# Kernel tuning notes

Hardware: AMD Instinct MI355X
Metric: run time of the kernel (lower is better)

Reference implementation:

```python
import jax, jax.numpy as jnp
import numpy as np

S = 3072      # total tokens across all images
DIM = 1280    # hidden_size
H = 16        # num_heads
HD = DIM // H # head_dim = 80
NSEG = 6      # number of images (cu_seqlens has NSEG+1 entries)


def _rotate_half(x):
    x1, x2 = jnp.split(x, 2, axis=-1)
    return jnp.concatenate([-x2, x1], axis=-1)


def setup_inputs() -> dict:
    key = jax.random.key(0)
    ks = jax.random.split(key, 12)
    hidden_states = jax.random.normal(ks[0], (S, DIM), jnp.float32)
    # realistic vision rotary embedding: half-dim inv_freq, repeated to head_dim
    inv_freq = 1.0 / (10000.0 ** (jnp.arange(0, HD // 2, dtype=jnp.float32) / (HD // 2)))
    freqs = jnp.arange(S, dtype=jnp.float32)[:, None] * inv_freq[None, :]  # [S, HD/2]
    emb = jnp.concatenate([freqs, freqs], axis=-1)  # [S, HD]
    cos = jnp.cos(emb)
    sin = jnp.sin(emb)
    sc = 0.02
    wq = jax.random.normal(ks[1], (DIM, DIM), jnp.float32) * sc
    bq = jax.random.normal(ks[2], (DIM,), jnp.float32) * sc
    wk = jax.random.normal(ks[3], (DIM, DIM), jnp.float32) * sc
    bk = jax.random.normal(ks[4], (DIM,), jnp.float32) * sc
    wv = jax.random.normal(ks[5], (DIM, DIM), jnp.float32) * sc
    bv = jax.random.normal(ks[6], (DIM,), jnp.float32) * sc
    wo = jax.random.normal(ks[7], (DIM, DIM), jnp.float32) * sc
    bo = jax.random.normal(ks[8], (DIM,), jnp.float32) * sc
    cu_seqlens = (jnp.arange(NSEG + 1, dtype=jnp.int32) * (S // NSEG))  # [0,512,...,3072]
    return dict(hidden_states=hidden_states, cos=cos, sin=sin,
                wq=wq, bq=bq, wk=wk, bk=bk, wv=wv, bv=bv, wo=wo, bo=bo,
                cu_seqlens=cu_seqlens)


def reference(hidden_states, cos, sin, wq, bq, wk, bk, wv, bv, wo, bo, cu_seqlens):
    seq_length = hidden_states.shape[0]
    scaling = HD ** (-0.5)
    # QKV projections (torch Linear: x @ W.T + b)
    q = (hidden_states @ wq.T + bq).reshape(seq_length, H, HD)
    k = (hidden_states @ wk.T + bk).reshape(seq_length, H, HD)
    v = (hidden_states @ wv.T + bv).reshape(seq_length, H, HD)
    # apply_rotary_pos_emb_vision: cos/sin [S, HD] broadcast over head axis
    c = cos[:, None, :]
    s = sin[:, None, :]
    q = q * c + _rotate_half(q) * s
    k = k * c + _rotate_half(k) * s
    # block-diagonal (per-image) attention via segment mask
    seg = jnp.searchsorted(cu_seqlens[1:], jnp.arange(seq_length), side='right')
    mask = seg[:, None] == seg[None, :]  # [S, S] bool
    scores = jnp.einsum('shd,thd->hst', q, k) * scaling  # [H, S, S]
    scores = jnp.where(mask[None, :, :], scores, jnp.finfo(scores.dtype).min)
    attn = jax.nn.softmax(scores, axis=-1)
    out = jnp.einsum('hst,thd->shd', attn, v).reshape(seq_length, DIM)
    return out @ wo.T + bo
```

## Files before the change

kernel.cpp:

```cpp
#include <hip/hip_runtime.h>
#include <hip/hip_bf16.h>
#include <hip/hip_fp16.h>
#include <cstdint>
#include <cstddef>

typedef _Float16 f16;
typedef f16 f16x2 __attribute__((ext_vector_type(2)));
typedef f16 f16x4 __attribute__((ext_vector_type(4)));
typedef f16 f16x8 __attribute__((ext_vector_type(8)));
typedef float f32x4 __attribute__((ext_vector_type(4)));

#define S_LEN 3072
#define DIM 1280
#define NH 16
#define HD 80
#define SEG 512

#define MFMA16F(a, b, c) __builtin_amdgcn_mfma_f32_16x16x32_f16((a), (b), (c), 0, 0, 0)

__device__ __forceinline__ void gl2lds16(const void* g, void* l) {
    __builtin_amdgcn_global_load_lds(
        (const __attribute__((address_space(1))) unsigned int*)g,
        (__attribute__((address_space(3))) unsigned int*)l, 16, 0, 0);
}

__device__ __forceinline__ unsigned int pack2(float a, float b) {
    f16x2 t = {(f16)a, (f16)b};
    union { f16x2 v; unsigned int u; } c;
    c.v = t;
    return c.u;
}

__global__ __launch_bounds__(256) void cvt_kernel(
    const float* __restrict__ hs,
    const float* __restrict__ wq, const float* __restrict__ wk,
    const float* __restrict__ wv, const float* __restrict__ wo,
    f16* __restrict__ hs16,
    f16* __restrict__ wq16, f16* __restrict__ wk16,
    f16* __restrict__ wv16, f16* __restrict__ wo16)
{
    const int m = blockIdx.y;
    const float* src; f16* dst; int n4;
    if (m == 0)      { src = hs; dst = hs16; n4 = S_LEN * DIM / 4; }
    else if (m == 1) { src = wq; dst = wq16; n4 = DIM * DIM / 4; }
    else if (m == 2) { src = wk; dst = wk16; n4 = DIM * DIM / 4; }
    else if (m == 3) { src = wv; dst = wv16; n4 = DIM * DIM / 4; }
    else             { src = wo; dst = wo16; n4 = DIM * DIM / 4; }
    int idx = blockIdx.x * 256 + threadIdx.x;
    if (idx >= n4) return;
    f32x4 v = *(const f32x4*)(src + (size_t)idx * 4);
    f16x4 o;
#pragma unroll
    for (int e = 0; e < 4; ++e) o[e] = (f16)v[e];
    *(f16x4*)(dst + (size_t)idx * 4) = o;
}

__global__ __launch_bounds__(512, 2) void gemm_qkv192(
    const f16* __restrict__ A, const f16* __restrict__ Wb,
    const float* __restrict__ bq, const float* __restrict__ bk,
    const float* __restrict__ bv,
    f16* __restrict__ q16, f16* __restrict__ k16, f16* __restrict__ vT)
{
    const int bid = blockIdx.x;
    const int xcd = bid & 7;
    const int idx = bid >> 3;
    const int mt = xcd * 2 + idx / 15;
    const int nt = idx % 15;
    const int m0 = mt * 192;
    const int n0 = nt * 256;

    __shared__ __align__(16) f16 Abuf[2][192 * 64];
    __shared__ __align__(16) f16 Bbuf[2][256 * 64];

    const int tid = threadIdx.x;
    const int w = tid >> 6;
    const int lane = tid & 63;
    const int lane15 = lane & 15;
    const int quad = lane >> 4;
    const int wm = (w >> 2) * 96;
    const int wn = (w & 3) * 64;

    const int srow = lane >> 3;
    const int schk = (lane & 7) ^ srow;

    const int aRow = w * 24;
    const int bRow = (w & 3) * 64 + (w >> 2) * 16;

    const f16* gA = A + (size_t)(m0 + aRow + srow) * DIM + schk * 8;
    const f16* gB = Wb + (size_t)(n0 + bRow + srow) * DIM + schk * 8;

    const int x7 = lane15 & 7;
    const int cc0 = (quad ^ x7) * 8;
    const int cc1 = ((quad + 4) ^ x7) * 8;

    f32x4 acc[6][4];
#pragma unroll
    for (int i = 0; i < 6; ++i)
#pragma unroll
        for (int j = 0; j < 4; ++j)
            acc[i][j] = (f32x4){0.f, 0.f, 0.f, 0.f};

    {
        f16* lB = Bbuf[0] + bRow * 64;
        gl2lds16(gB, lB);
        gl2lds16(gB + 8 * DIM, lB + 512);
        gl2lds16(gB + 32 * DIM, lB + 2048);
        gl2lds16(gB + 40 * DIM, lB + 2560);
        f16* lA = Abuf[0] + aRow * 64;
        gl2lds16(gA, lA);
        gl2lds16(gA + 8 * DIM, lA + 512);
        gl2lds16(gA + 16 * DIM, lA + 1024);
        f16* lB1 = Bbuf[1] + bRow * 64;
        gl2lds16(gB + 64, lB1);
        gl2lds16(gB + 8 * DIM + 64, lB1 + 512);
        gl2lds16(gB + 32 * DIM + 64, lB1 + 2048);
        gl2lds16(gB + 40 * DIM + 64, lB1 + 2560);
        f16* lA1 = Abuf[1] + aRow * 64;
        gl2lds16(gA + 64, lA1);
        gl2lds16(gA + 8 * DIM + 64, lA1 + 512);
        gl2lds16(gA + 16 * DIM + 64, lA1 + 1024);
    }
    asm volatile("s_waitcnt vmcnt(7)" ::: "memory");
    __builtin_amdgcn_s_barrier();

    f16x8 a0[3][2], a1[3][2], b01[2][2], b23[2][2];
#pragma unroll
    for (int i = 0; i < 3; ++i) {
        const f16* rp = Abuf[0] + (wm + i * 16 + lane15) * 64;
        a0[i][0] = *(const f16x8*)(rp + cc0);
        a0[i][1] = *(const f16x8*)(rp + cc1);
    }
#pragma unroll
    for (int j = 0; j < 2; ++j) {
        const f16* rp = Bbuf[0] + (wn + j * 16 + lane15) * 64;
        b01[j][0] = *(const f16x8*)(rp + cc0);
        b01[j][1] = *(const f16x8*)(rp + cc1);
    }

    for (int kt = 0; kt < 20; ++kt) {
        const int s = kt & 1;
        const int sn = s ^ 1;
        const int k2 = (kt + 2 < 20) ? kt + 2 : 19;
        const f16* As = Abuf[s];
        const f16* Bsl = Bbuf[s];
        const f16* Asn = Abuf[sn];
        const f16* Bsn = Bbuf[sn];
        const f16* gA2 = gA + k2 * 64;
        const f16* gB2 = gB + k2 * 64;

        __builtin_amdgcn_s_barrier();
        asm volatile("s_waitcnt lgkmcnt(0)" ::: "memory");
        __builtin_amdgcn_sched_barrier(0);
        __builtin_amdgcn_s_setprio(1);
#pragma unroll
        for (int i = 0; i < 3; ++i)
#pragma unroll
            for (int j = 0; j < 2; ++j) {
                acc[i][j] = MFMA16F(a0[i][0], b01[j][0], acc[i][j]);
                acc[i][j] = MFMA16F(a0[i][1], b01[j][1], acc[i][j]);
            }
        __builtin_amdgcn_s_setprio(0);
        __builtin_amdgcn_sched_barrier(0);
#pragma unroll
        for (int j = 0; j < 2; ++j) {
            const f16* rp = Bsl + (wn + 32 + j * 16 + lane15) * 64;
            b23[j][0] = *(const f16x8*)(rp + cc0);
            b23[j][1] = *(const f16x8*)(rp + cc1);
        }

        __builtin_amdgcn_s_barrier();
        asm volatile("s_waitcnt lgkmcnt(0)" ::: "memory");
        __builtin_amdgcn_sched_barrier(0);
        __builtin_amdgcn_s_setprio(1);
#pragma unroll
        for (int i = 0; i < 3; ++i)
#pragma unroll
            for (int j = 0; j < 2; ++j) {
                acc[i][j + 2] = MFMA16F(a0[i][0], b23[j][0], acc[i][j + 2]);
                acc[i][j + 2] = MFMA16F(a0[i][1], b23[j][1], acc[i][j + 2]);
            }
        __builtin_amdgcn_s_setprio(0);
        __builtin_amdgcn_sched_barrier(0);
#pragma unroll
        for (int i = 0; i < 3; ++i) {
            const f16* rp = As + (wm + 48 + i * 16 + lane15) * 64;
            a1[i][0] = *(const f16x8*)(rp + cc0);
            a1[i][1] = *(const f16x8*)(rp + cc1);
        }
        {
            f16* lB = Bbuf[s] + bRow * 64;
            gl2lds16(gB2, lB);
            gl2lds16(gB2 + 8 * DIM, lB + 512);
            gl2lds16(gB2 + 32 * DIM, lB + 2048);
            gl2lds16(gB2 + 40 * DIM, lB + 2560);
        }
        asm volatile("s_waitcnt vmcnt(4)" ::: "memory");

        __builtin_amdgcn_s_barrier();
        asm volatile("s_waitcnt lgkmcnt(0)" ::: "memory");
        __builtin_amdgcn_sched_barrier(0);
        __builtin_amdgcn_s_setprio(1);
#pragma unroll
        for (int i = 0; i < 3; ++i)
#pragma unroll
            for (int j = 0; j < 2; ++j) {
                acc[i + 3][j + 2] = MFMA16F(a1[i][0], b23[j][0], acc[i + 3][j + 2]);
                acc[i + 3][j + 2] = MFMA16F(a1[i][1], b23[j][1], acc[i + 3][j + 2]);
            }
        __builtin_amdgcn_s_setprio(0);
        __builtin_amdgcn_sched_barrier(0);
#pragma unroll
        for (int i = 0; i < 3; ++i) {
            const f16* rp = Asn + (wm + i * 16 + lane15) * 64;
            a0[i][0] = *(const f16x8*)(rp + cc0);
            a0[i][1] = *(const f16x8*)(rp + cc1);
        }
        {
            f16* lA = Abuf[s] + aRow * 64;
            gl2lds16(gA2, lA);
            gl2lds16(gA2 + 8 * DIM, lA + 512);
            gl2lds16(gA2 + 16 * DIM, lA + 1024);
        }

        __builtin_amdgcn_s_barrier();
        asm volatile("s_waitcnt lgkmcnt(0)" ::: "memory");
        __builtin_amdgcn_sched_barrier(0);
        __builtin_amdgcn_s_setprio(1);
#pragma unroll
        for (int i = 0; i < 3; ++i)
#pragma unroll
            for (int j = 0; j < 2; ++j) {
                acc[i + 3][j] = MFMA16F(a1[i][0], b01[j][0], acc[i + 3][j]);
                acc[i + 3][j] = MFMA16F(a1[i][1], b01[j][1], acc[i + 3][j]);
            }
        __builtin_amdgcn_s_setprio(0);
        __builtin_amdgcn_sched_barrier(0);
#pragma unroll
        for (int j = 0; j < 2; ++j) {
            const f16* rp = Bsn + (wn + j * 16 + lane15) * 64;
            b01[j][0] = *(const f16x8*)(rp + cc0);
            b01[j][1] = *(const f16x8*)(rp + cc1);
        }
    }
    asm volatile("s_waitcnt vmcnt(0) lgkmcnt(0)" ::: "memory");

    const int sel = nt / 5;
    const int nc0 = (nt % 5) * 256 + wn;
    const float* bias = (sel == 0) ? bq : (sel == 1) ? bk : bv;
    float bvv[4];
#pragma unroll
    for (int j = 0; j < 4; ++j) bvv[j] = bias[nc0 + j * 16 + lane15];

    if (sel < 2) {
        f16* O = sel ? k16 : q16;
#pragma unroll
        for (int i = 0; i < 6; ++i)
#pragma unroll
            for (int j = 0; j < 4; ++j)
#pragma unroll
                for (int r = 0; r < 4; ++r) {
                    int row = m0 + wm + i * 16 + quad * 4 + r;
                    O[(size_t)row * DIM + nc0 + j * 16 + lane15] =
                        (f16)(acc[i][j][r] + bvv[j]);
                }
    } else {
#pragma unroll
        for (int i = 0; i < 6; ++i)
#pragma unroll
            for (int j = 0; j < 4; ++j) {
                f16x4 ov;
#pragma unroll
                for (int r = 0; r < 4; ++r) ov[r] = (f16)(acc[i][j][r] + bvv[j]);
                int row = m0 + wm + i * 16 + quad * 4;
                int col = nc0 + j * 16 + lane15;
                *(f16x4*)(vT + (size_t)col * S_LEN + row) = ov;
            }
    }
}

__global__ __launch_bounds__(256, 2) void gemm_out_kernel(
    const f16* __restrict__ A, const f16* __restrict__ W,
    const float* __restrict__ bias, float* __restrict__ OF)
{
    const int bid = blockIdx.x;
    const int xcd = bid & 7;
    const int idx = bid >> 3;
    const int mt = xcd * 3 + idx / 10;
    const int nt = idx % 10;
    const int m0 = mt * 128;
    const int n0 = nt * 128;

    __shared__ __align__(16) f16 Abuf[2][128 * 64];
    __shared__ __align__(16) f16 Bbuf[2][128 * 64];

    const int tid = threadIdx.x;
    const int w = tid >> 6;
    const int lane = tid & 63;
    const int lane15 = lane & 15;
    const int quad = lane >> 4;
    const int wm = (w >> 1) * 64;
    const int wn = (w & 1) * 64;

    const int srow = lane >> 3;
    const int schk = (lane & 7) ^ srow;

    const int aRow = w * 32;
    const int bRow = w * 32;

    const f16* gA = A + (size_t)(m0 + aRow + srow) * DIM + schk * 8;
    const f16* gB = W + (size_t)(n0 + bRow + srow) * DIM + schk * 8;

    const int x7 = lane15 & 7;
    const int cc0 = (quad ^ x7) * 8;
    const int cc1 = ((quad + 4) ^ x7) * 8;

    f32x4 acc[4][4];
#pragma unroll
    for (int i = 0; i < 4; ++i)
#pragma unroll
        for (int j = 0; j < 4; ++j)
            acc[i][j] = (f32x4){0.f, 0.f, 0.f, 0.f};

    {
        f16* lB = Bbuf[0] + bRow * 64;
        gl2lds16(gB, lB);
        gl2lds16(gB + 8 * DIM, lB + 512);
        gl2lds16(gB + 16 * DIM, lB + 1024);
        gl2lds16(gB + 24 * DIM, lB + 1536);
        f16* lA = Abuf[0] + aRow * 64;
        gl2lds16(gA, lA);
        gl2lds16(gA + 8 * DIM, lA + 512);
        gl2lds16(gA + 16 * DIM, lA + 1024);
        gl2lds16(gA + 24 * DIM, lA + 1536);
        f16* lB1 = Bbuf[1] + bRow * 64;
        gl2lds16(gB + 64, lB1);
        gl2lds16(gB + 8 * DIM + 64, lB1 + 512);
        gl2lds16(gB + 16 * DIM + 64, lB1 + 1024);
        gl2lds16(gB + 24 * DIM + 64, lB1 + 1536);
        f16* lA1 = Abuf[1] + aRow * 64;
        gl2lds16(gA + 64, lA1);
        gl2lds16(gA + 8 * DIM + 64, lA1 + 512);
        gl2lds16(gA + 16 * DIM + 64, lA1 + 1024);
        gl2lds16(gA + 24 * DIM + 64, lA1 + 1536);
    }
    asm volatile("s_waitcnt vmcnt(8)" ::: "memory");
    __builtin_amdgcn_s_barrier();

    f16x8 a0[2][2], a1[2][2], b01[2][2], b23[2][2];
#pragma unroll
    for (int i = 0; i < 2; ++i) {
        const f16* rp = Abuf[0] + (wm + i * 16 + lane15) * 64;
        a0[i][0] = *(const f16x8*)(rp + cc0);
        a0[i][1] = *(const f16x8*)(rp + cc1);
    }
#pragma unroll
    for (int j = 0; j < 2; ++j) {
        const f16* rp = Bbuf[0] + (wn + j * 16 + lane15) * 64;
        b01[j][0] = *(const f16x8*)(rp + cc0);
        b01[j][1] = *(const f16x8*)(rp + cc1);
    }

    for (int kt = 0; kt < 20; ++kt) {
        const int s = kt & 1;
        const int sn = s ^ 1;
        const int k2 = (kt + 2 < 20) ? kt + 2 : 19;
        const f16* As = Abuf[s];
        const f16* Bsl = Bbuf[s];
        const f16* Asn = Abuf[sn];
        const f16* Bsn = Bbuf[sn];
        const f16* gA2 = gA + k2 * 64;
        const f16* gB2 = gB + k2 * 64;

        __builtin_amdgcn_s_barrier();
        asm volatile("s_waitcnt lgkmcnt(0)" ::: "memory");
        __builtin_amdgcn_sched_barrier(0);
        __builtin_amdgcn_s_setprio(1);
#pragma unroll
        for (int i = 0; i < 2; ++i)
#pragma unroll
            for (int j = 0; j < 2; ++j) {
                acc[i][j] = MFMA16F(a0[i][0], b01[j][0], acc[i][j]);
                acc[i][j] = MFMA16F(a0[i][1], b01[j][1], acc[i][j]);
            }
        __builtin_amdgcn_s_setprio(0);
        __builtin_amdgcn_sched_barrier(0);
#pragma unroll
        for (int j = 0; j < 2; ++j) {
            const f16* rp = Bsl + (wn + 32 + j * 16 + lane15) * 64;
            b23[j][0] = *(const f16x8*)(rp + cc0);
            b23[j][1] = *(const f16x8*)(rp + cc1);
        }

        __builtin_amdgcn_s_barrier();
        asm volatile("s_waitcnt lgkmcnt(0)" ::: "memory");
        __builtin_amdgcn_sched_barrier(0);
        __builtin_amdgcn_s_setprio(1);
#pragma unroll
        for (int i = 0; i < 2; ++i)
#pragma unroll
            for (int j = 0; j < 2; ++j) {
                acc[i][j + 2] = MFMA16F(a0[i][0], b23[j][0], acc[i][j + 2]);
                acc[i][j + 2] = MFMA16F(a0[i][1], b23[j][1], acc[i][j + 2]);
            }
        __builtin_amdgcn_s_setprio(0);
        __builtin_amdgcn_sched_barrier(0);
#pragma unroll
        for (int i = 0; i < 2; ++i) {
            const f16* rp = As + (wm + 32 + i * 16 + lane15) * 64;
            a1[i][0] = *(const f16x8*)(rp + cc0);
            a1[i][1] = *(const f16x8*)(rp + cc1);
        }
        {
            f16* lB = Bbuf[s] + bRow * 64;
            gl2lds16(gB2, lB);
            gl2lds16(gB2 + 8 * DIM, lB + 512);
            gl2lds16(gB2 + 16 * DIM, lB + 1024);
            gl2lds16(gB2 + 24 * DIM, lB + 1536);
        }
        asm volatile("s_waitcnt vmcnt(4)" ::: "memory");

        __builtin_amdgcn_s_barrier();
        asm volatile("s_waitcnt lgkmcnt(0)" ::: "memory");
        __builtin_amdgcn_sched_barrier(0);
        __builtin_amdgcn_s_setprio(1);
#pragma unroll
        for (int i = 0; i < 2; ++i)
#pragma unroll
            for (int j = 0; j < 2; ++j) {
                acc[i + 2][j + 2] = MFMA16F(a1[i][0], b23[j][0], acc[i + 2][j + 2]);
                acc[i + 2][j + 2] = MFMA16F(a1[i][1], b23[j][1], acc[i + 2][j + 2]);
            }
        __builtin_amdgcn_s_setprio(0);
        __builtin_amdgcn_sched_barrier(0);
#pragma unroll
        for (int i = 0; i < 2; ++i) {
            const f16* rp = Asn + (wm + i * 16 + lane15) * 64;
            a0[i][0] = *(const f16x8*)(rp + cc0);
            a0[i][1] = *(const f16x8*)(rp + cc1);
        }
        {
            f16* lA = Abuf[s] + aRow * 64;
            gl2lds16(gA2, lA);
            gl2lds16(gA2 + 8 * DIM, lA + 512);
            gl2lds16(gA2 + 16 * DIM, lA + 1024);
            gl2lds16(gA2 + 24 * DIM, lA + 1536);
        }

        __builtin_amdgcn_s_barrier();
        asm volatile("s_waitcnt lgkmcnt(0)" ::: "memory");
        __builtin_amdgcn_sched_barrier(0);
        __builtin_amdgcn_s_setprio(1);
#pragma unroll
        for (int i = 0; i < 2; ++i)
#pragma unroll
            for (int j = 0; j < 2; ++j) {
                acc[i + 2][j] = MFMA16F(a1[i][0], b01[j][0], acc[i + 2][j]);
                acc[i + 2][j] = MFMA16F(a1[i][1], b01[j][1], acc[i + 2][j]);
            }
        __builtin_amdgcn_s_setprio(0);
        __builtin_amdgcn_sched_barrier(0);
#pragma unroll
        for (int j = 0; j < 2; ++j) {
            const f16* rp = Bsn + (wn + j * 16 + lane15) * 64;
            b01[j][0] = *(const f16x8*)(rp + cc0);
            b01[j][1] = *(const f16x8*)(rp + cc1);
        }
    }
    asm volatile("s_waitcnt vmcnt(0) lgkmcnt(0)" ::: "memory");

    float bvv[4];
#pragma unroll
    for (int j = 0; j < 4; ++j)
        bvv[j] = bias[n0 + wn + j * 16 + lane15];

#pragma unroll
    for (int i = 0; i < 4; ++i)
#pragma unroll
        for (int j = 0; j < 4; ++j)
#pragma unroll
            for (int r = 0; r < 4; ++r) {
                int row = m0 + wm + i * 16 + quad * 4 + r;
                int col = n0 + wn + j * 16 + lane15;
                OF[(size_t)row * DIM + col] = acc[i][j][r] + bvv[j];
            }
}

__global__ __launch_bounds__(256) void rope_kernel(
    f16* __restrict__ qb, f16* __restrict__ kb,
    const float* __restrict__ cosb, const float* __restrict__ sinb)
{
    int idx = blockIdx.x * 256 + threadIdx.x;
    int c = idx % 5;
    int t = idx / 5;
    int h = t & 15; t >>= 4;
    int s = t % S_LEN;
    int which = t / S_LEN;
    f16* buf = which ? kb : qb;
    float scale = which ? 1.0f : 0.11180339887498948f;
    int j = c * 8;
    f32x4 ca = *(const f32x4*)(cosb + s * HD + j);
    f32x4 cb = *(const f32x4*)(cosb + s * HD + j + 4);
    f32x4 sna = *(const f32x4*)(sinb + s * HD + j);
    f32x4 snb = *(const f32x4*)(sinb + s * HD + j + 4);
    size_t base = (size_t)s * DIM + h * HD + j;
    f16x8 x1 = *(f16x8*)(buf + base);
    f16x8 x2 = *(f16x8*)(buf + base + 40);
    f16x8 o1, o2;
#pragma unroll
    for (int e = 0; e < 8; ++e) {
        float ce = (e < 4) ? ca[e] : cb[e - 4];
        float se = (e < 4) ? sna[e] : snb[e - 4];
        float a = (float)x1[e], b = (float)x2[e];
        o1[e] = (f16)((a * ce - b * se) * scale);
        o2[e] = (f16)((b * ce + a * se) * scale);
    }
    *(f16x8*)(buf + base) = o1;
    *(f16x8*)(buf + base + 40) = o2;
}

__global__ __launch_bounds__(512, 4) void attn_kernel(
    const f16* __restrict__ q, const f16* __restrict__ k,
    const f16* __restrict__ vT, f16* __restrict__ o)
{
    const int h = blockIdx.x;
    const int g = blockIdx.y;
    const int qc = blockIdx.z;
    const int tid = threadIdx.x;
    const int lane15 = tid & 15;
    const int quad = (tid & 63) >> 4;
    const int w = tid >> 6;
    const int qbase = g * SEG + qc * 128;
    const int qrow = qbase + w * 16 + lane15;

    __shared__ __align__(16) f16 Ks2[10 * 128 * 8];
    __shared__ __align__(16) f16 Vt[80 * 128];

    f16x8 zf;
#pragma unroll
    for (int e = 0; e < 8; ++e) zf[e] = (f16)0.0f;

    f16x8 fq[3];
#pragma unroll
    for (int kc = 0; kc < 3; ++kc) {
        if (kc == 2 && quad >= 2) fq[kc] = zf;
        else fq[kc] = *(const f16x8*)(q + (size_t)qrow * DIM + h * HD + kc * 32 + quad * 8);
    }

    float m_run = -1e30f, l_run = 0.f;
    f32x4 Oa[5];
#pragma unroll
    for (int dt = 0; dt < 5; ++dt) Oa[dt] = (f32x4){0.f, 0.f, 0.f, 0.f};

    for (int kt = 0; kt < 4; ++kt) {
        __syncthreads();
        const int kb = g * SEG + kt * 128;
        for (int c = tid; c < 1280; c += 512) {
            int r = c / 10;
            int ch = c - r * 10;
            int rr = r ^ (ch & 7);
            *(f16x8*)(Ks2 + ch * 1024 + rr * 8) =
                *(const f16x8*)(k + (size_t)(kb + r) * DIM + h * HD + ch * 8);
        }
        for (int c = (tid ^ 256); c < 1280; c += 512) {
            int d = c >> 4;
            int sc = c & 15;
            *(f16x8*)(Vt + d * 128 + (sc ^ (d & 7)) * 8) =
                *(const f16x8*)(vT + (size_t)(h * HD + d) * S_LEN + kb + sc * 8);
        }
        __syncthreads();

        f32x4 sa[8];
#pragma unroll
        for (int nt = 0; nt < 8; ++nt) sa[nt] = (f32x4){0.f, 0.f, 0.f, 0.f};
#pragma unroll
        for (int kc = 0; kc < 3; ++kc) {
#pragma unroll
            for (int nt = 0; nt < 8; ++nt) {
                f16x8 fk;
                if (kc == 2 && quad >= 2) fk = zf;
                else {
                    int ch = kc * 4 + quad;
                    int rr = (nt * 16 + lane15) ^ (ch & 7);
                    fk = *(const f16x8*)(Ks2 + ch * 1024 + rr * 8);
                }
                sa[nt] = MFMA16F(fk, fq[kc], sa[nt]);
            }
        }

        float mt = -1e30f;
#pragma unroll
        for (int nt = 0; nt < 8; ++nt)
#pragma unroll
            for (int r = 0; r < 4; ++r) mt = fmaxf(mt, sa[nt][r]);
        mt = fmaxf(mt, __shfl_xor(mt, 16, 64));
        mt = fmaxf(mt, __shfl_xor(mt, 32, 64));

        float mn = fmaxf(m_run, mt);
        float alpha = __expf(m_run - mn);
        m_run = mn;
        float lt = 0.f;
        unsigned int pp[8][2];
#pragma unroll
        for (int nt = 0; nt < 8; ++nt) {
            float p0 = __expf(sa[nt][0] - mn);
            float p1 = __expf(sa[nt][1] - mn);
            float p2 = __expf(sa[nt][2] - mn);
            float p3 = __expf(sa[nt][3] - mn);
            lt += (p0 + p1) + (p2 + p3);
            pp[nt][0] = pack2(p0, p1);
            pp[nt][1] = pack2(p2, p3);
        }
        lt += __shfl_xor(lt, 16, 64);
        lt += __shfl_xor(lt, 32, 64);
        l_run = l_run * alpha + lt;

#pragma unroll
        for (int dt = 0; dt < 5; ++dt)
#pragma unroll
            for (int r = 0; r < 4; ++r) Oa[dt][r] *= alpha;

        const int srcA = ((quad & 1) * 2) * 16 + lane15;
        const int srcB = srcA + 16;
        const bool hi = quad >= 2;
#pragma unroll
        for (int kc2 = 0; kc2 < 4; ++kc2) {
            unsigned int e0 = __shfl((int)pp[2 * kc2][0], srcA, 64);
            unsigned int e1 = __shfl((int)pp[2 * kc2][1], srcA, 64);
            unsigned int e2 = __shfl((int)pp[2 * kc2][0], srcB, 64);
            unsigned int e3 = __shfl((int)pp[2 * kc2][1], srcB, 64);
            unsigned int o0 = __shfl((int)pp[2 * kc2 + 1][0], srcA, 64);
            unsigned int o1 = __shfl((int)pp[2 * kc2 + 1][1], srcA, 64);
            unsigned int o2 = __shfl((int)pp[2 * kc2 + 1][0], srcB, 64);
            unsigned int o3 = __shfl((int)pp[2 * kc2 + 1][1], srcB, 64);
            union { unsigned int u[4]; f16x8 v; } fp;
            fp.u[0] = hi ? o0 : e0;
            fp.u[1] = hi ? o1 : e1;
            fp.u[2] = hi ? o2 : e2;
            fp.u[3] = hi ? o3 : e3;
#pragma unroll
            for (int dt = 0; dt < 5; ++dt) {
                int drow = dt * 16 + lane15;
                int slot = (kc2 * 4 + quad) ^ (drow & 7);
                f16x8 fv = *(const f16x8*)(Vt + drow * 128 + slot * 8);
                Oa[dt] = MFMA16F(fv, fp.v, Oa[dt]);
            }
        }
    }

    float inv = 1.0f / l_run;
#pragma unroll
    for (int dt = 0; dt < 5; ++dt) {
        f16x4 ov;
#pragma unroll
        for (int r = 0; r < 4; ++r) ov[r] = (f16)(Oa[dt][r] * inv);
        *(f16x4*)(o + (size_t)qrow * DIM + h * HD + dt * 16 + quad * 4) = ov;
    }
}

extern "C" void kernel_launch(void* const* d_in, const int* in_sizes, int n_in,
                              void* d_out, int out_size, void* d_ws, size_t ws_size,
                              hipStream_t stream)
{
    const float* hs   = (const float*)d_in[0];
    const float* cosb = (const float*)d_in[1];
    const float* sinb = (const float*)d_in[2];
    const float* wq   = (const float*)d_in[3];
    const float* bq   = (const float*)d_in[4];
    const float* wk   = (const float*)d_in[5];
    const float* bk   = (const float*)d_in[6];
    const float* wv   = (const float*)d_in[7];
    const float* bv   = (const float*)d_in[8];
    const float* wo   = (const float*)d_in[9];
    const float* bo   = (const float*)d_in[10];

    const size_t SD = (size_t)S_LEN * DIM;
    const size_t WW = (size_t)DIM * DIM;
    f16* hs16 = (f16*)d_ws;
    f16* wq16 = hs16 + SD;
    f16* wk16 = wq16 + WW;
    f16* wv16 = wk16 + WW;
    f16* wo16 = wv16 + WW;
    f16* q16  = wo16 + WW;
    f16* k16  = q16 + SD;
    f16* vT16 = k16 + SD;
    f16* ao16 = vT16 + SD;
    float* outb = (float*)d_out;

    cvt_kernel<<<dim3(S_LEN * DIM / 4 / 256, 5), 256, 0, stream>>>(
        hs, wq, wk, wv, wo, hs16, wq16, wk16, wv16, wo16);
    gemm_qkv192<<<240, 512, 0, stream>>>(
        hs16, wq16, bq, bk, bv, q16, k16, vT16);
    rope_kernel<<<1920, 256, 0, stream>>>(q16, k16, cosb, sinb);
    attn_kernel<<<dim3(NH, 6, 4), 512, 0, stream>>>(q16, k16, vT16, ao16);
    gemm_out_kernel<<<240, 256, 0, stream>>>(ao16, wo16, bo, outb);
}
```

Measured before the change: 195.3 us.

## Retile QKV GEMM to 128x192 blocks and compact cvt kernel grid

```diff
diff --git a/kernel.cpp b/kernel.cpp
--- a/kernel.cpp
+++ b/kernel.cpp
@@ -39,23 +39,27 @@
     f16* __restrict__ wq16, f16* __restrict__ wk16,
     f16* __restrict__ wv16, f16* __restrict__ wo16)
 {
-    const int m = blockIdx.y;
-    const float* src; f16* dst; int n4;
-    if (m == 0)      { src = hs; dst = hs16; n4 = S_LEN * DIM / 4; }
-    else if (m == 1) { src = wq; dst = wq16; n4 = DIM * DIM / 4; }
-    else if (m == 2) { src = wk; dst = wk16; n4 = DIM * DIM / 4; }
-    else if (m == 3) { src = wv; dst = wv16; n4 = DIM * DIM / 4; }
-    else             { src = wo; dst = wo16; n4 = DIM * DIM / 4; }
-    int idx = blockIdx.x * 256 + threadIdx.x;
-    if (idx >= n4) return;
-    f32x4 v = *(const f32x4*)(src + (size_t)idx * 4);
+    int b = blockIdx.x;
+    const float* src; f16* dst; size_t gi;
+    if (b < 3840) {
+        src = hs; dst = hs16;
+        gi = (size_t)b * 256 + threadIdx.x;
+    } else {
+        int t = b - 3840;
+        int m = t / 1600;
+        int bi = t - m * 1600;
+        src = (m == 0) ? wq : (m == 1) ? wk : (m == 2) ? wv : wo;
+        dst = (m == 0) ? wq16 : (m == 1) ? wk16 : (m == 2) ? wv16 : wo16;
+        gi = (size_t)bi * 256 + threadIdx.x;
+    }
+    f32x4 v = *(const f32x4*)(src + gi * 4);
     f16x4 o;
 #pragma unroll
     for (int e = 0; e < 4; ++e) o[e] = (f16)v[e];
-    *(f16x4*)(dst + (size_t)idx * 4) = o;
-}
-
-__global__ __launch_bounds__(512, 2) void gemm_qkv192(
+    *(f16x4*)(dst + gi * 4) = o;
+}
+
+__global__ __launch_bounds__(512, 4) void gemm_qkv128(
     const f16* __restrict__ A, const f16* __restrict__ Wb,
     const float* __restrict__ bq, const float* __restrict__ bk,
     const float* __restrict__ bv,
@@ -64,27 +68,27 @@
     const int bid = blockIdx.x;
     const int xcd = bid & 7;
     const int idx = bid >> 3;
-    const int mt = xcd * 2 + idx / 15;
-    const int nt = idx % 15;
-    const int m0 = mt * 192;
-    const int n0 = nt * 256;
-
-    __shared__ __align__(16) f16 Abuf[2][192 * 64];
-    __shared__ __align__(16) f16 Bbuf[2][256 * 64];
+    const int mt = xcd * 3 + idx / 20;
+    const int nt = idx % 20;
+    const int m0 = mt * 128;
+    const int n0 = nt * 192;
+
+    __shared__ __align__(16) f16 Abuf[2][128 * 64];
+    __shared__ __align__(16) f16 Bbuf[2][192 * 64];
 
     const int tid = threadIdx.x;
     const int w = tid >> 6;
     const int lane = tid & 63;
     const int lane15 = lane & 15;
     const int quad = lane >> 4;
-    const int wm = (w >> 2) * 96;
-    const int wn = (w & 3) * 64;
+    const int wm = (w >> 2) * 64;
+    const int wn = (w & 3) * 48;
 
     const int srow = lane >> 3;
     const int schk = (lane & 7) ^ srow;
 
-    const int aRow = w * 24;
-    const int bRow = (w & 3) * 64 + (w >> 2) * 16;
+    const int aRow = w * 16;
+    const int bRow = w * 24;
 
     const f16* gA = A + (size_t)(m0 + aRow + srow) * DIM + schk * 8;
     const f16* gB = Wb + (size_t)(n0 + bRow + srow) * DIM + schk * 8;
@@ -93,48 +97,44 @@
     const int cc0 = (quad ^ x7) * 8;
     const int cc1 = ((quad + 4) ^ x7) * 8;
 
-    f32x4 acc[6][4];
-#pragma unroll
-    for (int i = 0; i < 6; ++i)
-#pragma unroll
-        for (int j = 0; j < 4; ++j)
+    f32x4 acc[4][3];
+#pragma unroll
+    for (int i = 0; i < 4; ++i)
+#pragma unroll
+        for (int j = 0; j < 3; ++j)
             acc[i][j] = (f32x4){0.f, 0.f, 0.f, 0.f};
 
     {
         f16* lB = Bbuf[0] + bRow * 64;
         gl2lds16(gB, lB);
         gl2lds16(gB + 8 * DIM, lB + 512);
-        gl2lds16(gB + 32 * DIM, lB + 2048);
-        gl2lds16(gB + 40 * DIM, lB + 2560);
+        gl2lds16(gB + 16 * DIM, lB + 1024);
         f16* lA = Abuf[0] + aRow * 64;
         gl2lds16(gA, lA);
         gl2lds16(gA + 8 * DIM, lA + 512);
-        gl2lds16(gA + 16 * DIM, lA + 1024);
         f16* lB1 = Bbuf[1] + bRow * 64;
         gl2lds16(gB + 64, lB1);
         gl2lds16(gB + 8 * DIM + 64, lB1 + 512);
-        gl2lds16(gB + 32 * DIM + 64, lB1 + 2048);
-        gl2lds16(gB + 40 * DIM + 64, lB1 + 2560);
+        gl2lds16(gB + 16 * DIM + 64, lB1 + 1024);
         f16* lA1 = Abuf[1] + aRow * 64;
         gl2lds16(gA + 64, lA1);
         gl2lds16(gA + 8 * DIM + 64, lA1 + 512);
-        gl2lds16(gA + 16 * DIM + 64, lA1 + 1024);
-    }
-    asm volatile("s_waitcnt vmcnt(7)" ::: "memory");
+    }
+    asm volatile("s_waitcnt vmcnt(5)" ::: "memory");
     __builtin_amdgcn_s_barrier();
 
-    f16x8 a0[3][2], a1[3][2], b01[2][2], b23[2][2];
-#pragma unroll
-    for (int i = 0; i < 3; ++i) {
+    f16x8 aLo[2][2], aHi[2][2], b[3][2];
+#pragma unroll
+    for (int j = 0; j < 3; ++j) {
+        const f16* rp = Bbuf[0] + (wn + j * 16 + lane15) * 64;
+        b[j][0] = *(const f16x8*)(rp + cc0);
+        b[j][1] = *(const f16x8*)(rp + cc1);
+    }
+#pragma unroll
+    for (int i = 0; i < 2; ++i) {
         const f16* rp = Abuf[0] + (wm + i * 16 + lane15) * 64;
-        a0[i][0] = *(const f16x8*)(rp + cc0);
-        a0[i][1] = *(const f16x8*)(rp + cc1);
-    }
-#pragma unroll
-    for (int j = 0; j < 2; ++j) {
-        const f16* rp = Bbuf[0] + (wn + j * 16 + lane15) * 64;
-        b01[j][0] = *(const f16x8*)(rp + cc0);
-        b01[j][1] = *(const f16x8*)(rp + cc1);
+        aLo[i][0] = *(const f16x8*)(rp + cc0);
+        aLo[i][1] = *(const f16x8*)(rp + cc1);
     }
 
     for (int kt = 0; kt < 20; ++kt) {
@@ -142,7 +142,6 @@
         const int sn = s ^ 1;
         const int k2 = (kt + 2 < 20) ? kt + 2 : 19;
         const f16* As = Abuf[s];
-        const f16* Bsl = Bbuf[s];
         const f16* Asn = Abuf[sn];
         const f16* Bsn = Bbuf[sn];
         const f16* gA2 = gA + k2 * 64;
@@ -153,128 +152,89 @@
         __builtin_amdgcn_sched_barrier(0);
         __builtin_amdgcn_s_setprio(1);
 #pragma unroll
-        for (int i = 0; i < 3; ++i)
-#pragma unroll
-            for (int j = 0; j < 2; ++j) {
-                acc[i][j] = MFMA16F(a0[i][0], b01[j][0], acc[i][j]);
-                acc[i][j] = MFMA16F(a0[i][1], b01[j][1], acc[i][j]);
+        for (int i = 0; i < 2; ++i)
+#pragma unroll
+            for (int j = 0; j < 3; ++j) {
+                acc[i][j] = MFMA16F(aLo[i][0], b[j][0], acc[i][j]);
+                acc[i][j] = MFMA16F(aLo[i][1], b[j][1], acc[i][j]);
             }
         __builtin_amdgcn_s_setprio(0);
         __builtin_amdgcn_sched_barrier(0);
-#pragma unroll
-        for (int j = 0; j < 2; ++j) {
-            const f16* rp = Bsl + (wn + 32 + j * 16 + lane15) * 64;
-            b23[j][0] = *(const f16x8*)(rp + cc0);
-            b23[j][1] = *(const f16x8*)(rp + cc1);
-        }
-
-        __builtin_amdgcn_s_barrier();
-        asm volatile("s_waitcnt lgkmcnt(0)" ::: "memory");
-        __builtin_amdgcn_sched_barrier(0);
-        __builtin_amdgcn_s_setprio(1);
-#pragma unroll
-        for (int i = 0; i < 3; ++i)
-#pragma unroll
-            for (int j = 0; j < 2; ++j) {
-                acc[i][j + 2] = MFMA16F(a0[i][0], b23[j][0], acc[i][j + 2]);
-                acc[i][j + 2] = MFMA16F(a0[i][1], b23[j][1], acc[i][j + 2]);
-            }
-        __builtin_amdgcn_s_setprio(0);
-        __builtin_amdgcn_sched_barrier(0);
-#pragma unroll
-        for (int i = 0; i < 3; ++i) {
-            const f16* rp = As + (wm + 48 + i * 16 + lane15) * 64;
-            a1[i][0] = *(const f16x8*)(rp + cc0);
-            a1[i][1] = *(const f16x8*)(rp + cc1);
-        }
         {
             f16* lB = Bbuf[s] + bRow * 64;
             gl2lds16(gB2, lB);
             gl2lds16(gB2 + 8 * DIM, lB + 512);
-            gl2lds16(gB2 + 32 * DIM, lB + 2048);
-            gl2lds16(gB2 + 40 * DIM, lB + 2560);
-        }
-        asm volatile("s_waitcnt vmcnt(4)" ::: "memory");
+            gl2lds16(gB2 + 16 * DIM, lB + 1024);
+        }
+        asm volatile("s_waitcnt vmcnt(3)" ::: "memory");
+#pragma unroll
+        for (int i = 0; i < 2; ++i) {
+            const f16* rp = As + (wm + (i + 2) * 16 + lane15) * 64;
+            aHi[i][0] = *(const f16x8*)(rp + cc0);
+            aHi[i][1] = *(const f16x8*)(rp + cc1);
+        }
 
         __builtin_amdgcn_s_barrier();
         asm volatile("s_waitcnt lgkmcnt(0)" ::: "memory");
         __builtin_amdgcn_sched_barrier(0);
         __builtin_amdgcn_s_setprio(1);
 #pragma unroll
-        for (int i = 0; i < 3; ++i)
-#pragma unroll
-            for (int j = 0; j < 2; ++j) {
-                acc[i + 3][j + 2] = MFMA16F(a1[i][0], b23[j][0], acc[i + 3][j + 2]);
-                acc[i + 3][j + 2] = MFMA16F(a1[i][1], b23[j][1], acc[i + 3][j + 2]);
+        for (int i = 0; i < 2; ++i)
+#pragma unroll
+            for (int j = 0; j < 3; ++j) {
+                acc[i + 2][j] = MFMA16F(aHi[i][0], b[j][0], acc[i + 2][j]);
+                acc[i + 2][j] = MFMA16F(aHi[i][1], b[j][1], acc[i + 2][j]);
             }
         __builtin_amdgcn_s_setprio(0);
         __builtin_amdgcn_sched_barrier(0);
-#pragma unroll
-        for (int i = 0; i < 3; ++i) {
-            const f16* rp = Asn + (wm + i * 16 + lane15) * 64;
-            a0[i][0] = *(const f16x8*)(rp + cc0);
-            a0[i][1] = *(const f16x8*)(rp + cc1);
-        }
         {
             f16* lA = Abuf[s] + aRow * 64;
             gl2lds16(gA2, lA);
             gl2lds16(gA2 + 8 * DIM, lA + 512);
-            gl2lds16(gA2 + 16 * DIM, lA + 1024);
-        }
-
-        __builtin_amdgcn_s_barrier();
-        asm volatile("s_waitcnt lgkmcnt(0)" ::: "memory");
-        __builtin_amdgcn_sched_barrier(0);
-        __builtin_amdgcn_s_setprio(1);
-#pragma unroll
-        for (int i = 0; i < 3; ++i)
-#pragma unroll
-            for (int j = 0; j < 2; ++j) {
-                acc[i + 3][j] = MFMA16F(a1[i][0], b01[j][0], acc[i + 3][j]);
-                acc[i + 3][j] = MFMA16F(a1[i][1], b01[j][1], acc[i + 3][j]);
-            }
-        __builtin_amdgcn_s_setprio(0);
-        __builtin_amdgcn_sched_barrier(0);
-#pragma unroll
-        for (int j = 0; j < 2; ++j) {
+        }
+#pragma unroll
+        for (int j = 0; j < 3; ++j) {
             const f16* rp = Bsn + (wn + j * 16 + lane15) * 64;
-            b01[j][0] = *(const f16x8*)(rp + cc0);
-            b01[j][1] = *(const f16x8*)(rp + cc1);
+            b[j][0] = *(const f16x8*)(rp + cc0);
+            b[j][1] = *(const f16x8*)(rp + cc1);
+        }
+#pragma unroll
+        for (int i = 0; i < 2; ++i) {
+            const f16* rp = Asn + (wm + i * 16 + lane15) * 64;
+            aLo[i][0] = *(const f16x8*)(rp + cc0);
+            aLo[i][1] = *(const f16x8*)(rp + cc1);
         }
     }
     asm volatile("s_waitcnt vmcnt(0) lgkmcnt(0)" ::: "memory");
 
-    const int sel = nt / 5;
-    const int nc0 = (nt % 5) * 256 + wn;
-    const float* bias = (sel == 0) ? bq : (sel == 1) ? bk : bv;
-    float bvv[4];
-#pragma unroll
-    for (int j = 0; j < 4; ++j) bvv[j] = bias[nc0 + j * 16 + lane15];
-
-    if (sel < 2) {
-        f16* O = sel ? k16 : q16;
-#pragma unroll
-        for (int i = 0; i < 6; ++i)
-#pragma unroll
-            for (int j = 0; j < 4; ++j)
+#pragma unroll
+    for (int j = 0; j < 3; ++j) {
+        const int ncj = n0 + wn + j * 16;
+        if (ncj < 2560) {
+            f16* O = (ncj < 1280) ? q16 : k16;
+            const float* bb = (ncj < 1280) ? bq : bk;
+            const int cb = (ncj < 1280) ? ncj : ncj - 1280;
+            float bv_ = bb[cb + lane15];
+#pragma unroll
+            for (int i = 0; i < 4; ++i)
 #pragma unroll
                 for (int r = 0; r < 4; ++r) {
                     int row = m0 + wm + i * 16 + quad * 4 + r;
-                    O[(size_t)row * DIM + nc0 + j * 16 + lane15] =
-                        (f16)(acc[i][j][r] + bvv[j]);
+                    O[(size_t)row * DIM + cb + lane15] =
+                        (f16)(acc[i][j][r] + bv_);
                 }
-    } else {
-#pragma unroll
-        for (int i = 0; i < 6; ++i)
-#pragma unroll
-            for (int j = 0; j < 4; ++j) {
+        } else {
+            const int cb = ncj - 2560;
+            float bv_ = bv[cb + lane15];
+#pragma unroll
+            for (int i = 0; i < 4; ++i) {
                 f16x4 ov;
 #pragma unroll
-                for (int r = 0; r < 4; ++r) ov[r] = (f16)(acc[i][j][r] + bvv[j]);
+                for (int r = 0; r < 4; ++r) ov[r] = (f16)(acc[i][j][r] + bv_);
                 int row = m0 + wm + i * 16 + quad * 4;
-                int col = nc0 + j * 16 + lane15;
-                *(f16x4*)(vT + (size_t)col * S_LEN + row) = ov;
-            }
+                *(f16x4*)(vT + (size_t)(cb + lane15) * S_LEN + row) = ov;
+            }
+        }
     }
 }
 
@@ -686,9 +646,9 @@
     f16* ao16 = vT16 + SD;
     float* outb = (float*)d_out;
 
-    cvt_kernel<<<dim3(S_LEN * DIM / 4 / 256, 5), 256, 0, stream>>>(
+    cvt_kernel<<<3840 + 4 * 1600, 256, 0, stream>>>(
         hs, wq, wk, wv, wo, hs16, wq16, wk16, wv16, wo16);
-    gemm_qkv192<<<240, 512, 0, stream>>>(
+    gemm_qkv128<<<480, 512, 0, stream>>>(
         hs16, wq16, bq, bk, bv, q16, k16, vT16);
     rope_kernel<<<1920, 256, 0, stream>>>(q16, k16, cosb, sinb);
     attn_kernel<<<dim3(NH, 6, 4), 512, 0, stream>>>(q16, k16, vT16, ao16);
```

Result: no change. 196.3 us (+0.5%).

## Double-buffer attention K/V tiles via async global-to-LDS loads; compact cvt grid

Applied to the files above, without the earlier changes.

```diff
diff --git a/kernel.cpp b/kernel.cpp
--- a/kernel.cpp
+++ b/kernel.cpp
@@ -39,20 +39,24 @@
     f16* __restrict__ wq16, f16* __restrict__ wk16,
     f16* __restrict__ wv16, f16* __restrict__ wo16)
 {
-    const int m = blockIdx.y;
-    const float* src; f16* dst; int n4;
-    if (m == 0)      { src = hs; dst = hs16; n4 = S_LEN * DIM / 4; }
-    else if (m == 1) { src = wq; dst = wq16; n4 = DIM * DIM / 4; }
-    else if (m == 2) { src = wk; dst = wk16; n4 = DIM * DIM / 4; }
-    else if (m == 3) { src = wv; dst = wv16; n4 = DIM * DIM / 4; }
-    else             { src = wo; dst = wo16; n4 = DIM * DIM / 4; }
-    int idx = blockIdx.x * 256 + threadIdx.x;
-    if (idx >= n4) return;
-    f32x4 v = *(const f32x4*)(src + (size_t)idx * 4);
+    int b = blockIdx.x;
+    const float* src; f16* dst; size_t gi;
+    if (b < 3840) {
+        src = hs; dst = hs16;
+        gi = (size_t)b * 256 + threadIdx.x;
+    } else {
+        int t = b - 3840;
+        int m = t / 1600;
+        int bi = t - m * 1600;
+        src = (m == 0) ? wq : (m == 1) ? wk : (m == 2) ? wv : wo;
+        dst = (m == 0) ? wq16 : (m == 1) ? wk16 : (m == 2) ? wv16 : wo16;
+        gi = (size_t)bi * 256 + threadIdx.x;
+    }
+    f32x4 v = *(const f32x4*)(src + gi * 4);
     f16x4 o;
 #pragma unroll
     for (int e = 0; e < 4; ++e) o[e] = (f16)v[e];
-    *(f16x4*)(dst + (size_t)idx * 4) = o;
+    *(f16x4*)(dst + gi * 4) = o;
 }
 
 __global__ __launch_bounds__(512, 2) void gemm_qkv192(
@@ -526,14 +530,36 @@
     const int g = blockIdx.y;
     const int qc = blockIdx.z;
     const int tid = threadIdx.x;
+    const int lane = tid & 63;
     const int lane15 = tid & 15;
     const int quad = (tid & 63) >> 4;
     const int w = tid >> 6;
     const int qbase = g * SEG + qc * 128;
     const int qrow = qbase + w * 16 + lane15;
 
-    __shared__ __align__(16) f16 Ks2[10 * 128 * 8];
-    __shared__ __align__(16) f16 Vt[80 * 128];
+    __shared__ __align__(16) f16 Ks2[2][10 * 128 * 8];
+    __shared__ __align__(16) f16 Vt[2][80 * 128];
+
+#define STAGE_KV(kb_, dst)                                                    \
+    if (w < 4) {                                                              \
+        _Pragma("unroll")                                                     \
+        for (int sgi = 0; sgi < 5; ++sgi) {                                   \
+            int i_ = w * 5 + sgi;                                             \
+            int ch_ = i_ >> 1, half_ = i_ & 1;                                \
+            int r_ = (half_ * 64 + lane) ^ (ch_ & 7);                         \
+            gl2lds16(k + (size_t)((kb_) + r_) * DIM + h * HD + ch_ * 8,       \
+                     Ks2[dst] + ch_ * 1024 + half_ * 512);                    \
+        }                                                                     \
+    } else {                                                                  \
+        _Pragma("unroll")                                                     \
+        for (int sgi = 0; sgi < 5; ++sgi) {                                   \
+            int j_ = (w - 4) * 5 + sgi;                                       \
+            int d_ = j_ * 4 + (lane >> 4);                                    \
+            int sc_ = (lane & 15) ^ (d_ & 7);                                 \
+            gl2lds16(vT + (size_t)(h * HD + d_) * S_LEN + (kb_) + sc_ * 8,    \
+                     Vt[dst] + j_ * 512);                                     \
+        }                                                                     \
+    }
 
     f16x8 zf;
 #pragma unroll
@@ -551,23 +577,15 @@
 #pragma unroll
     for (int dt = 0; dt < 5; ++dt) Oa[dt] = (f32x4){0.f, 0.f, 0.f, 0.f};
 
+    STAGE_KV(g * SEG, 0);
+    asm volatile("s_waitcnt vmcnt(0)" ::: "memory");
+    __builtin_amdgcn_s_barrier();
+
     for (int kt = 0; kt < 4; ++kt) {
-        __syncthreads();
-        const int kb = g * SEG + kt * 128;
-        for (int c = tid; c < 1280; c += 512) {
-            int r = c / 10;
-            int ch = c - r * 10;
-            int rr = r ^ (ch & 7);
-            *(f16x8*)(Ks2 + ch * 1024 + rr * 8) =
-                *(const f16x8*)(k + (size_t)(kb + r) * DIM + h * HD + ch * 8);
-        }
-        for (int c = (tid ^ 256); c < 1280; c += 512) {
-            int d = c >> 4;
-            int sc = c & 15;
-            *(f16x8*)(Vt + d * 128 + (sc ^ (d & 7)) * 8) =
-                *(const f16x8*)(vT + (size_t)(h * HD + d) * S_LEN + kb + sc * 8);
-        }
-        __syncthreads();
+        const int b = kt & 1;
+        if (kt < 3) { STAGE_KV(g * SEG + (kt + 1) * 128, b ^ 1); }
+        const f16* Kb = Ks2[b];
+        const f16* Vb = Vt[b];
 
         f32x4 sa[8];
 #pragma unroll
@@ -581,7 +599,7 @@
                 else {
                     int ch = kc * 4 + quad;
                     int rr = (nt * 16 + lane15) ^ (ch & 7);
-                    fk = *(const f16x8*)(Ks2 + ch * 1024 + rr * 8);
+                    fk = *(const f16x8*)(Kb + ch * 1024 + rr * 8);
                 }
                 sa[nt] = MFMA16F(fk, fq[kc], sa[nt]);
             }
@@ -641,11 +659,15 @@
             for (int dt = 0; dt < 5; ++dt) {
                 int drow = dt * 16 + lane15;
                 int slot = (kc2 * 4 + quad) ^ (drow & 7);
-                f16x8 fv = *(const f16x8*)(Vt + drow * 128 + slot * 8);
+                f16x8 fv = *(const f16x8*)(Vb + drow * 128 + slot * 8);
                 Oa[dt] = MFMA16F(fv, fp.v, Oa[dt]);
             }
         }
-    }
+
+        asm volatile("s_waitcnt vmcnt(0)" ::: "memory");
+        __syncthreads();
+    }
+#undef STAGE_KV
 
     float inv = 1.0f / l_run;
 #pragma unroll
@@ -686,7 +708,7 @@
     f16* ao16 = vT16 + SD;
     float* outb = (float*)d_out;
 
-    cvt_kernel<<<dim3(S_LEN * DIM / 4 / 256, 5), 256, 0, stream>>>(
+    cvt_kernel<<<3840 + 4 * 1600, 256, 0, stream>>>(
         hs, wq, wk, wv, wo, hs16, wq16, wk16, wv16, wo16);
     gemm_qkv192<<<240, 512, 0, stream>>>(
         hs16, wq16, bq, bk, bv, q16, k16, vT16);
```

Result: slower. 205.6 us (+5.3%).
